# Kernel optimization log

Measured on AMD Instinct MI355X. Metric: run time of the kernel, lower is better.

Reference implementation:

```python
import jax, jax.numpy as jnp
import numpy as np

N_NODES = 20000
N_EDGES = 320000
NODE_DIM = 512
HIDDEN = 512
N_GRAPHS = 64


def setup_inputs() -> dict:
    key = jax.random.key(0)
    ks = jax.random.split(key, 12)
    s = 0.02
    return {
        "joint_x": jax.random.normal(ks[0], (N_NODES, NODE_DIM), jnp.float32),
        "joint_edge_index": jax.random.randint(ks[1], (2, N_EDGES), 0, N_NODES, dtype=jnp.int32),
        "joint_batch": jnp.sort(jax.random.randint(ks[2], (N_NODES,), 0, N_GRAPHS, dtype=jnp.int32)),
        "W_g1": jax.random.normal(ks[3], (NODE_DIM, HIDDEN), jnp.float32) * s,
        "b_g1": jnp.zeros((HIDDEN,), jnp.float32),
        "W_g2": jax.random.normal(ks[4], (HIDDEN, HIDDEN), jnp.float32) * s,
        "b_g2": jnp.zeros((HIDDEN,), jnp.float32),
        "W_c1": jax.random.normal(ks[5], (HIDDEN, HIDDEN // 2), jnp.float32) * s,
        "b_c1": jnp.zeros((HIDDEN // 2,), jnp.float32),
        "W_c2": jax.random.normal(ks[6], (HIDDEN // 2, 1), jnp.float32) * s,
        "b_c2": jnp.zeros((1,), jnp.float32),
    }


def _gin_layer(h, src, dst, W, b):
    # GINConv(nn=Linear, eps=0): nn((1+eps)*x_i + sum_{j->i} x_j)
    agg = jax.ops.segment_sum(h[src], dst, num_segments=N_NODES)  # [N, D]
    return (h + agg) @ W + b


def reference(joint_x, joint_edge_index, joint_batch, W_g1, b_g1, W_g2, b_g2, W_c1, b_c1, W_c2, b_c2):
    src, dst = joint_edge_index[0], joint_edge_index[1]
    h = _gin_layer(joint_x, src, dst, W_g1, b_g1)  # [N, HIDDEN]
    h = _gin_layer(h, src, dst, W_g2, b_g2)        # [N, HIDDEN]
    pooled = jax.ops.segment_sum(h, joint_batch, num_segments=N_GRAPHS)  # [G, HIDDEN]
    z = jax.nn.relu(pooled @ W_c1 + b_c1)
    score = z @ W_c2 + b_c2                        # [G, 1]
    return jax.nn.sigmoid(score).squeeze(-1)       # [G]
```

## Files before the change

### kernel.cpp

```cpp
#include <hip/hip_runtime.h>
#include <math.h>

constexpr int N_NODES = 20000;
constexpr int DIM = 512;
constexpr int NG = 64;
constexpr int CAP = 64;
constexpr int KCH = 80;
constexpr int NCHUNK = (N_NODES + KCH - 1) / KCH;
constexpr int RSPLIT = 10;
constexpr int CPS = (NCHUNK + RSPLIT - 1) / RSPLIT;
constexpr int CGS = 32;
constexpr int CSTR = 16;
constexpr int NODE_BLOCKS = (N_NODES + 3) / 4;
constexpr int INIT_BLOCKS = (N_NODES + 255) / 256;
constexpr int GEMM_TILES = 17 * 4;
constexpr int KSPLIT_TILES = GEMM_TILES * 2;
constexpr int PQ_ELEMS = 513 * 256;
constexpr int EPT = 2;
constexpr int EDGE_BLOCKS = (320000 + 256 * EPT - 1) / (256 * EPT);

__device__ __forceinline__ int lower_bound_i(const int* __restrict__ a, int n, int v) {
  int lo = 0, hi = n;
  while (lo < hi) {
    int mid = (lo + hi) >> 1;
    if (a[mid] < v) lo = mid + 1; else hi = mid;
  }
  return lo;
}

__global__ __launch_bounds__(256) void node_init(const int* __restrict__ batch,
                                                 int* __restrict__ cursor,
                                                 float* __restrict__ ng,
                                                 float* __restrict__ cgpad, int n_nodes) {
  int node = blockIdx.x * 256 + threadIdx.x;
  if (node < n_nodes) cursor[(size_t)node * CSTR] = 0;
  if (blockIdx.x == 0 && threadIdx.x < 64) {
    int gg = threadIdx.x;
    int s0 = lower_bound_i(batch, n_nodes, gg);
    int e0 = lower_bound_i(batch, n_nodes, gg + 1);
    ng[gg] = (float)(e0 - s0);
    cgpad[gg * CGS] = 0.f;
  }
}

__device__ void gemm_stack_tile(const float* __restrict__ A0, const float* __restrict__ extra,
                                const float* __restrict__ B, const float* __restrict__ B2,
                                float* __restrict__ C,
                                int N, int K, int R0, int tile, int kbeg, int kend,
                                float* As, float* Bs, int tid) {
  int bm = (tile >> 2) * 32;
  int bn = (tile & 3) * 64;
  int tx = tid & 15;
  int ty = tid >> 4;
  int ar = tid >> 3;
  int ac = (tid & 7) * 2;
  int br = tid >> 4;
  int bc = (tid & 15) * 4;
  float acc[2][4] = {};
  for (int k0 = kbeg; k0 < kend; k0 += 16) {
    int row = bm + ar;
    float2 av = make_float2(0.f, 0.f);
    if (row < R0)       av = *(const float2*)(A0 + (size_t)row * K + k0 + ac);
    else if (row == R0) av = *(const float2*)(extra + k0 + ac);
    As[(ac + 0) * 34 + ar] = av.x;
    As[(ac + 1) * 34 + ar] = av.y;
    size_t boff = (size_t)(k0 + br) * N + bn + bc;
    float4 bv = *(const float4*)(B + boff);
    if (B2) {
      float4 b2 = *(const float4*)(B2 + boff);
      bv.x += b2.x; bv.y += b2.y; bv.z += b2.z; bv.w += b2.w;
    }
    *(float4*)&Bs[br * 68 + bc] = bv;
    __syncthreads();
#pragma unroll
    for (int kk = 0; kk < 16; ++kk) {
      float2 a01 = *(const float2*)&As[kk * 34 + ty * 2];
      float4 b4  = *(const float4*)&Bs[kk * 68 + tx * 4];
      acc[0][0] = fmaf(a01.x, b4.x, acc[0][0]); acc[0][1] = fmaf(a01.x, b4.y, acc[0][1]);
      acc[0][2] = fmaf(a01.x, b4.z, acc[0][2]); acc[0][3] = fmaf(a01.x, b4.w, acc[0][3]);
      acc[1][0] = fmaf(a01.y, b4.x, acc[1][0]); acc[1][1] = fmaf(a01.y, b4.y, acc[1][1]);
      acc[1][2] = fmaf(a01.y, b4.z, acc[1][2]); acc[1][3] = fmaf(a01.y, b4.w, acc[1][3]);
    }
    __syncthreads();
  }
#pragma unroll
  for (int i = 0; i < 2; ++i) {
    int m = bm + ty * 2 + i;
    if (m > R0) continue;
    *(float4*)&C[(size_t)m * N + bn + tx * 4] =
        make_float4(acc[i][0], acc[i][1], acc[i][2], acc[i][3]);
  }
}

__global__ __launch_bounds__(256) void fill_and_Q(const int* __restrict__ srcI,
                                                  const int* __restrict__ dstI,
                                                  const int* __restrict__ batch,
                                                  int* __restrict__ cursor,
                                                  int* __restrict__ edst,
                                                  float* __restrict__ cgpad,
                                                  const float* __restrict__ Wg2,
                                                  const float* __restrict__ bg2,
                                                  const float* __restrict__ Wc1,
                                                  float* __restrict__ Q, int n_edges) {
  __shared__ float As[16 * 34];
  __shared__ float Bs[16 * 68];
  __shared__ int hist[64];
  int b = blockIdx.x;
  int t = threadIdx.x;
  if (b < KSPLIT_TILES) {
    int ks = b & 1;
    int tile = b >> 1;
    gemm_stack_tile(Wg2, bg2, Wc1, nullptr, Q + (size_t)ks * PQ_ELEMS,
                    256, 512, 512, tile, ks * 256, ks * 256 + 256, As, Bs, t);
  } else {
    int eb = b - KSPLIT_TILES;
    if (t < 64) hist[t] = 0;
    __syncthreads();
    int base = eb * (256 * EPT) + t;
    int s[EPT], d[EPT], c[EPT];
    bool v[EPT];
#pragma unroll
    for (int u = 0; u < EPT; ++u) {
      int i = base + u * 256;
      v[u] = i < n_edges;
      s[u] = v[u] ? srcI[i] : 0;
    }
#pragma unroll
    for (int u = 0; u < EPT; ++u) {
      int i = base + u * 256;
      d[u] = v[u] ? dstI[i] : 0;
    }
#pragma unroll
    for (int u = 0; u < EPT; ++u)
      if (v[u]) c[u] = atomicAdd(&cursor[(size_t)s[u] * CSTR], 1);
#pragma unroll
    for (int u = 0; u < EPT; ++u)
      if (v[u]) edst[(size_t)s[u] * CAP + c[u]] = d[u];
#pragma unroll
    for (int u = 0; u < EPT; ++u)
      if (v[u]) atomicAdd(&hist[batch[d[u]]], 1);
    __syncthreads();
    if (t < 64 && hist[t] != 0) atomicAdd(&cgpad[t * CGS], (float)hist[t]);
  }
}

__global__ __launch_bounds__(256) void wT_and_P(const int* __restrict__ batch,
                                                const int* __restrict__ deg,
                                                const int* __restrict__ edst,
                                                float* __restrict__ wT,
                                                const float* __restrict__ Wg1,
                                                const float* __restrict__ bg1,
                                                const float* __restrict__ Q,
                                                float* __restrict__ P, int n_nodes) {
  __shared__ float As[16 * 34];
  __shared__ float Bs[16 * 68];
  int b = blockIdx.x;
  int t = threadIdx.x;
  if (b < KSPLIT_TILES) {
    int ks = b & 1;
    int tile = b >> 1;
    gemm_stack_tile(Wg1, bg1, Q, Q + PQ_ELEMS, P + (size_t)ks * PQ_ELEMS,
                    256, 512, 512, tile, ks * 256, ks * 256 + 256, As, Bs, t);
  } else {
    int node = (b - KSPLIT_TILES) * 4 + (t >> 6);
    int g = t & 63;
    if (node >= n_nodes) return;
    int end = deg[(size_t)node * CSTR];
    const int* nb = edst + (size_t)node * CAP;
    float acc = (batch[node] == g) ? 1.f : 0.f;
    int i = 0;
    for (; i + 7 < end; i += 8) {
      int d0 = nb[i], d1 = nb[i + 1], d2 = nb[i + 2], d3 = nb[i + 3];
      int d4 = nb[i + 4], d5 = nb[i + 5], d6 = nb[i + 6], d7 = nb[i + 7];
      int b0 = batch[d0], b1 = batch[d1], b2 = batch[d2], b3 = batch[d3];
      int b4 = batch[d4], b5 = batch[d5], b6 = batch[d6], b7 = batch[d7];
      acc += ((float)(b0 == g) + (float)(b1 == g)) + ((float)(b2 == g) + (float)(b3 == g)) +
             ((float)(b4 == g) + (float)(b5 == g)) + ((float)(b6 == g) + (float)(b7 == g));
    }
    for (; i < end; ++i) acc += (float)(batch[nb[i]] == g);
    wT[(size_t)node * 64 + g] = acc;
  }
}

__global__ __launch_bounds__(512) void ct_ugemm(const float* __restrict__ wT,
                                                const int* __restrict__ deg,
                                                const int* __restrict__ edst,
                                                const float* __restrict__ x,
                                                float* __restrict__ Upart, int n_nodes) {
  __shared__ float scT[KCH][64];
  int c = blockIdx.x;
  int t = threadIdx.x;
  int w = t >> 6;
  int g = t & 63;
  int k0 = c * KCH;
  int kmax = (n_nodes - k0) < KCH ? (n_nodes - k0) : KCH;
  for (int i = w; i < kmax; i += 8) {
    int node = k0 + i;
    float acc = wT[(size_t)node * 64 + g];
    int end = deg[(size_t)node * CSTR];
    const int* nb = edst + (size_t)node * CAP;
    int j = 0;
    for (; j + 7 < end; j += 8) {
      int d0 = nb[j], d1 = nb[j + 1], d2 = nb[j + 2], d3 = nb[j + 3];
      int d4 = nb[j + 4], d5 = nb[j + 5], d6 = nb[j + 6], d7 = nb[j + 7];
      float v0 = wT[(size_t)d0 * 64 + g], v1 = wT[(size_t)d1 * 64 + g];
      float v2 = wT[(size_t)d2 * 64 + g], v3 = wT[(size_t)d3 * 64 + g];
      float v4 = wT[(size_t)d4 * 64 + g], v5 = wT[(size_t)d5 * 64 + g];
      float v6 = wT[(size_t)d6 * 64 + g], v7 = wT[(size_t)d7 * 64 + g];
      acc += ((v0 + v1) + (v2 + v3)) + ((v4 + v5) + (v6 + v7));
    }
    for (; j + 3 < end; j += 4) {
      int d0 = nb[j], d1 = nb[j + 1], d2 = nb[j + 2], d3 = nb[j + 3];
      acc += wT[(size_t)d0 * 64 + g] + wT[(size_t)d1 * 64 + g] +
             wT[(size_t)d2 * 64 + g] + wT[(size_t)d3 * 64 + g];
    }
    for (; j < end; ++j) acc += wT[(size_t)nb[j] * 64 + g];
    scT[i][g] = acc;
  }
  __syncthreads();
  const float2* x2 = (const float2*)x;
  float2 acc[8][4];
#pragma unroll
  for (int q = 0; q < 8; ++q)
#pragma unroll
    for (int u = 0; u < 4; ++u) acc[q][u] = make_float2(0.f, 0.f);
#pragma unroll 2
  for (int kk = 0; kk < kmax; ++kk) {
    float2 xv[4];
#pragma unroll
    for (int u = 0; u < 4; ++u)
      xv[u] = x2[(size_t)(k0 + kk) * 256 + g + u * 64];
    const float4* cp = (const float4*)&scT[kk][w * 8];
    float4 cA = cp[0], cB = cp[1];
    float cv[8] = {cA.x, cA.y, cA.z, cA.w, cB.x, cB.y, cB.z, cB.w};
#pragma unroll
    for (int q = 0; q < 8; ++q)
#pragma unroll
      for (int u = 0; u < 4; ++u) {
        acc[q][u].x = fmaf(cv[q], xv[u].x, acc[q][u].x);
        acc[q][u].y = fmaf(cv[q], xv[u].y, acc[q][u].y);
      }
  }
  float2* up = (float2*)Upart;
#pragma unroll
  for (int q = 0; q < 8; ++q) {
    int gg = w * 8 + q;
#pragma unroll
    for (int u = 0; u < 4; ++u)
      up[((size_t)c * 64 + gg) * 256 + g + u * 64] = acc[q][u];
  }
}

__global__ __launch_bounds__(128) void reduce_U(const float* __restrict__ Upart,
                                                float* __restrict__ Ured) {
  int g = blockIdx.x;
  int s = blockIdx.y;
  int t = threadIdx.x;
  int c0 = s * CPS;
  int c1 = (c0 + CPS < NCHUNK) ? c0 + CPS : NCHUNK;
  const float4* up = (const float4*)Upart;
  float4 acc = make_float4(0.f, 0.f, 0.f, 0.f);
  for (int c = c0; c < c1; ++c) {
    float4 v = up[((size_t)c * 64 + g) * 128 + t];
    acc.x += v.x; acc.y += v.y; acc.z += v.z; acc.w += v.w;
  }
  ((float4*)Ured)[((size_t)s * 64 + g) * 128 + t] = acc;
}

__global__ __launch_bounds__(256) void head(const float* __restrict__ Ured,
                                            const float* __restrict__ P,
                                            const float* __restrict__ Q,
                                            const float* __restrict__ ng,
                                            const float* __restrict__ cgpad,
                                            const float* __restrict__ bc1,
                                            const float* __restrict__ Wc2,
                                            const float* __restrict__ bc2,
                                            float* __restrict__ out) {
  int g = blockIdx.x;
  int j = threadIdx.x;
  const float* Wc0 = P;
  const float* Wc1p = P + (size_t)PQ_ELEMS;
  const float* v1a = P + (size_t)512 * 256;
  const float* v1b = P + (size_t)PQ_ELEMS + (size_t)512 * 256;
  const float* v2a = Q + (size_t)512 * 256;
  const float* v2b = Q + (size_t)PQ_ELEMS + (size_t)512 * 256;
  __shared__ float p[512];
  float s0 = 0.f, s1 = 0.f;
#pragma unroll
  for (int s = 0; s < RSPLIT; ++s) {
    s0 += Ured[((size_t)s * 64 + g) * DIM + j];
    s1 += Ured[((size_t)s * 64 + g) * DIM + 256 + j];
  }
  p[j] = s0;
  p[j + 256] = s1;
  __syncthreads();
  float cg = ng[g] + cgpad[g * CGS];
  float acc = bc1[j] + cg * (v1a[j] + v1b[j]) + ng[g] * (v2a[j] + v2b[j]);
  for (int k = 0; k < 512; ++k) {
    float w = Wc0[k * 256 + j] + Wc1p[k * 256 + j];
    acc = fmaf(p[k], w, acc);
  }
  float z = fmaxf(acc, 0.f);
  float part = z * Wc2[j];
  for (int off = 32; off > 0; off >>= 1) part += __shfl_down(part, off, 64);
  __shared__ float red[4];
  if ((j & 63) == 0) red[j >> 6] = part;
  __syncthreads();
  if (j == 0) {
    float tot = red[0] + red[1] + red[2] + red[3] + bc2[0];
    out[g] = 1.f / (1.f + expf(-tot));
  }
}

extern "C" void kernel_launch(void* const* d_in, const int* in_sizes, int n_in,
                              void* d_out, int out_size, void* d_ws, size_t ws_size,
                              hipStream_t stream) {
  const float* x    = (const float*)d_in[0];
  const int*   ei   = (const int*)d_in[1];
  const int*   batch= (const int*)d_in[2];
  const float* Wg1  = (const float*)d_in[3];
  const float* bg1  = (const float*)d_in[4];
  const float* Wg2  = (const float*)d_in[5];
  const float* bg2  = (const float*)d_in[6];
  const float* Wc1  = (const float*)d_in[7];
  const float* bc1  = (const float*)d_in[8];
  const float* Wc2  = (const float*)d_in[9];
  const float* bc2  = (const float*)d_in[10];
  float* out = (float*)d_out;

  int n_edges = in_sizes[1] / 2;
  int n_nodes = in_sizes[2];
  const int* srcI = ei;
  const int* dstI = ei + n_edges;

  char* ws = (char*)d_ws;
  size_t off = 0;
  auto alloc = [&](size_t bytes) { char* p = ws + off; off += (bytes + 255) & ~(size_t)255; return p; };
  float* wT    = (float*)alloc((size_t)N_NODES * 64 * sizeof(float));
  float* Upart = (float*)alloc((size_t)NCHUNK * 64 * DIM * sizeof(float));
  float* Ured  = (float*)alloc((size_t)RSPLIT * 64 * DIM * sizeof(float));
  float* Q     = (float*)alloc((size_t)2 * PQ_ELEMS * sizeof(float));
  float* P     = (float*)alloc((size_t)2 * PQ_ELEMS * sizeof(float));
  float* ng    = (float*)alloc(NG * sizeof(float));
  float* cgpad = (float*)alloc(NG * CGS * sizeof(float));
  int* cursor  = (int*)alloc((size_t)N_NODES * CSTR * sizeof(int));
  int* edst    = (int*)alloc((size_t)N_NODES * CAP * sizeof(int));

  node_init<<<INIT_BLOCKS, 256, 0, stream>>>(batch, cursor, ng, cgpad, n_nodes);
  fill_and_Q<<<KSPLIT_TILES + EDGE_BLOCKS, 256, 0, stream>>>(srcI, dstI, batch, cursor, edst,
                                                             cgpad, Wg2, bg2, Wc1, Q, n_edges);
  wT_and_P<<<KSPLIT_TILES + NODE_BLOCKS, 256, 0, stream>>>(batch, cursor, edst, wT,
                                                           Wg1, bg1, Q, P, n_nodes);
  ct_ugemm<<<NCHUNK, 512, 0, stream>>>(wT, cursor, edst, x, Upart, n_nodes);
  reduce_U<<<dim3(64, RSPLIT), 128, 0, stream>>>(Upart, Ured);
  head<<<NG, 256, 0, stream>>>(Ured, P, Q, ng, cgpad, bc1, Wc2, bc2, out);
}
```

Before: 239.4 us.

## Split ct_ugemm columns across two blocks and double-buffer x loads

Launches ct_ugemm on a 2D grid so that each of the 250 node chunks is handled by two blocks, each computing half of the 512 output columns. This gives more blocks to fill the GPU and halves the per-thread accumulator registers. The GEMM loop is restructured to prefetch x rows four at a time into alternating register buffers, overlapping global loads with FMAs, and launch_bounds now asks for 4 blocks per CU. In exchange, each block repeats the neighbour-gather that builds scT, so that gather work is duplicated. The loop also assumes kmax is a multiple of 8.

```diff
diff --git a/kernel.cpp b/kernel.cpp
--- a/kernel.cpp
+++ b/kernel.cpp
@@ -7,6 +7,7 @@
 constexpr int CAP = 64;
 constexpr int KCH = 80;
 constexpr int NCHUNK = (N_NODES + KCH - 1) / KCH;
+constexpr int NSPLIT = 2;
 constexpr int RSPLIT = 10;
 constexpr int CPS = (NCHUNK + RSPLIT - 1) / RSPLIT;
 constexpr int CGS = 32;
@@ -182,13 +183,36 @@
   }
 }
 
-__global__ __launch_bounds__(512) void ct_ugemm(const float* __restrict__ wT,
-                                                const int* __restrict__ deg,
-                                                const int* __restrict__ edst,
-                                                const float* __restrict__ x,
-                                                float* __restrict__ Upart, int n_nodes) {
+#define LOADX(X, KB)                                                      \
+  _Pragma("unroll")                                                       \
+  for (int t_ = 0; t_ < 4; ++t_) {                                        \
+    X[t_][0] = x2[(size_t)(k0 + (KB) + t_) * 256 + ncol];                 \
+    X[t_][1] = x2[(size_t)(k0 + (KB) + t_) * 256 + ncol + 64];            \
+  }
+
+#define COMPX(X, KB)                                                      \
+  _Pragma("unroll")                                                       \
+  for (int t_ = 0; t_ < 4; ++t_) {                                        \
+    const float4* cp_ = (const float4*)&scT[(KB) + t_][w * 8];            \
+    float4 cA_ = cp_[0], cB_ = cp_[1];                                    \
+    float cv_[8] = {cA_.x, cA_.y, cA_.z, cA_.w, cB_.x, cB_.y, cB_.z, cB_.w}; \
+    _Pragma("unroll")                                                     \
+    for (int q_ = 0; q_ < 8; ++q_) {                                      \
+      acc[q_][0].x = fmaf(cv_[q_], X[t_][0].x, acc[q_][0].x);             \
+      acc[q_][0].y = fmaf(cv_[q_], X[t_][0].y, acc[q_][0].y);             \
+      acc[q_][1].x = fmaf(cv_[q_], X[t_][1].x, acc[q_][1].x);             \
+      acc[q_][1].y = fmaf(cv_[q_], X[t_][1].y, acc[q_][1].y);             \
+    }                                                                     \
+  }
+
+__global__ __launch_bounds__(512, 4) void ct_ugemm(const float* __restrict__ wT,
+                                                   const int* __restrict__ deg,
+                                                   const int* __restrict__ edst,
+                                                   const float* __restrict__ x,
+                                                   float* __restrict__ Upart, int n_nodes) {
   __shared__ float scT[KCH][64];
-  int c = blockIdx.x;
+  int c = blockIdx.y;
+  int nx = blockIdx.x;
   int t = threadIdx.x;
   int w = t >> 6;
   int g = t & 63;
@@ -196,7 +220,7 @@
   int kmax = (n_nodes - k0) < KCH ? (n_nodes - k0) : KCH;
   for (int i = w; i < kmax; i += 8) {
     int node = k0 + i;
-    float acc = wT[(size_t)node * 64 + g];
+    float acc1 = wT[(size_t)node * 64 + g];
     int end = deg[(size_t)node * CSTR];
     const int* nb = edst + (size_t)node * CAP;
     int j = 0;
@@ -207,47 +231,39 @@
       float v2 = wT[(size_t)d2 * 64 + g], v3 = wT[(size_t)d3 * 64 + g];
       float v4 = wT[(size_t)d4 * 64 + g], v5 = wT[(size_t)d5 * 64 + g];
       float v6 = wT[(size_t)d6 * 64 + g], v7 = wT[(size_t)d7 * 64 + g];
-      acc += ((v0 + v1) + (v2 + v3)) + ((v4 + v5) + (v6 + v7));
+      acc1 += ((v0 + v1) + (v2 + v3)) + ((v4 + v5) + (v6 + v7));
     }
     for (; j + 3 < end; j += 4) {
       int d0 = nb[j], d1 = nb[j + 1], d2 = nb[j + 2], d3 = nb[j + 3];
-      acc += wT[(size_t)d0 * 64 + g] + wT[(size_t)d1 * 64 + g] +
-             wT[(size_t)d2 * 64 + g] + wT[(size_t)d3 * 64 + g];
-    }
-    for (; j < end; ++j) acc += wT[(size_t)nb[j] * 64 + g];
-    scT[i][g] = acc;
+      acc1 += wT[(size_t)d0 * 64 + g] + wT[(size_t)d1 * 64 + g] +
+              wT[(size_t)d2 * 64 + g] + wT[(size_t)d3 * 64 + g];
+    }
+    for (; j < end; ++j) acc1 += wT[(size_t)nb[j] * 64 + g];
+    scT[i][g] = acc1;
   }
   __syncthreads();
   const float2* x2 = (const float2*)x;
-  float2 acc[8][4];
-#pragma unroll
-  for (int q = 0; q < 8; ++q)
-#pragma unroll
-    for (int u = 0; u < 4; ++u) acc[q][u] = make_float2(0.f, 0.f);
-#pragma unroll 2
-  for (int kk = 0; kk < kmax; ++kk) {
-    float2 xv[4];
-#pragma unroll
-    for (int u = 0; u < 4; ++u)
-      xv[u] = x2[(size_t)(k0 + kk) * 256 + g + u * 64];
-    const float4* cp = (const float4*)&scT[kk][w * 8];
-    float4 cA = cp[0], cB = cp[1];
-    float cv[8] = {cA.x, cA.y, cA.z, cA.w, cB.x, cB.y, cB.z, cB.w};
-#pragma unroll
-    for (int q = 0; q < 8; ++q)
-#pragma unroll
-      for (int u = 0; u < 4; ++u) {
-        acc[q][u].x = fmaf(cv[q], xv[u].x, acc[q][u].x);
-        acc[q][u].y = fmaf(cv[q], xv[u].y, acc[q][u].y);
-      }
+  int ncol = nx * 128 + g;
+  float2 acc[8][2];
+#pragma unroll
+  for (int q = 0; q < 8; ++q) {
+    acc[q][0] = make_float2(0.f, 0.f);
+    acc[q][1] = make_float2(0.f, 0.f);
+  }
+  float2 xa[4][2], xb[4][2];
+  LOADX(xa, 0);
+  for (int kk = 0; kk < kmax; kk += 8) {
+    LOADX(xb, kk + 4);
+    COMPX(xa, kk);
+    if (kk + 8 < kmax) { LOADX(xa, kk + 8); }
+    COMPX(xb, kk + 4);
   }
   float2* up = (float2*)Upart;
 #pragma unroll
   for (int q = 0; q < 8; ++q) {
     int gg = w * 8 + q;
-#pragma unroll
-    for (int u = 0; u < 4; ++u)
-      up[((size_t)c * 64 + gg) * 256 + g + u * 64] = acc[q][u];
+    up[((size_t)c * 64 + gg) * 256 + ncol] = acc[q][0];
+    up[((size_t)c * 64 + gg) * 256 + ncol + 64] = acc[q][1];
   }
 }
 
@@ -351,7 +367,7 @@
                                                              cgpad, Wg2, bg2, Wc1, Q, n_edges);
   wT_and_P<<<KSPLIT_TILES + NODE_BLOCKS, 256, 0, stream>>>(batch, cursor, edst, wT,
                                                            Wg1, bg1, Q, P, n_nodes);
-  ct_ugemm<<<NCHUNK, 512, 0, stream>>>(wT, cursor, edst, x, Upart, n_nodes);
+  ct_ugemm<<<dim3(NSPLIT, NCHUNK), 512, 0, stream>>>(wT, cursor, edst, x, Upart, n_nodes);
   reduce_U<<<dim3(64, RSPLIT), 128, 0, stream>>>(Upart, Ured);
   head<<<NG, 256, 0, stream>>>(Ured, P, Q, ng, cgpad, bc1, Wc2, bc2, out);
 }
```

Measured after the change: 234.7 us. No clear change (-2.0%).
